# Optimization experiments

Hardware: AMD Instinct MI355X
Metric: run time of the kernel (lower is better)

## Reference

```python
import jax, jax.numpy as jnp
import numpy as np

B, S, E, H = 8, 1024, 1024, 16
D = E // H  # head_dim = 64


def setup_inputs() -> dict:
    key = jax.random.key(0)
    ks = jax.random.split(key, 8)
    scale = 1.0 / np.sqrt(E)
    return {
        "query": jax.random.normal(ks[0], (B, S, E), jnp.float32),
        "key": jax.random.normal(ks[1], (B, S, E), jnp.float32),
        "value": jax.random.normal(ks[2], (B, S, E), jnp.float32),
        "q_w": jax.random.normal(ks[3], (E, E), jnp.float32) * scale,
        "q_b": jnp.zeros((E,), jnp.float32),
        "k_w": jax.random.normal(ks[4], (E, E), jnp.float32) * scale,
        "k_b": jnp.zeros((E,), jnp.float32),
        "v_w": jax.random.normal(ks[5], (E, E), jnp.float32) * scale,
        "v_b": jnp.zeros((E,), jnp.float32),
        "out_w": jax.random.normal(ks[6], (E, E), jnp.float32) * scale,
        "out_b": jnp.zeros((E,), jnp.float32),
    }


def reference(query, key, value, q_w, q_b, k_w, k_b, v_w, v_b, out_w, out_b):
    b = query.shape[0]
    scaling = 1.0 / jnp.sqrt(jnp.asarray(D, query.dtype))
    # torch Linear: x @ W.T + b; split heads -> (b, H, S, D)
    def proj(x, w, bias):
        y = jnp.einsum('bse,fe->bsf', x, w) + bias
        return y.reshape(b, -1, H, D).transpose(0, 2, 1, 3)
    q = proj(query, q_w, q_b)
    k = proj(key, k_w, k_b)
    v = proj(value, v_w, v_b)
    scores = jnp.einsum('bhqd,bhkd->bhqk', q, k) * scaling
    attn_weights = jax.nn.softmax(scores, axis=-1)
    # dropout is identity in eval mode (deterministic reference)
    context = jnp.einsum('bhqk,bhkd->bhqd', attn_weights, v)
    context = context.transpose(0, 2, 1, 3).reshape(b, -1, E)
    output = jnp.einsum('bse,fe->bsf', context, out_w) + out_b
    return (attn_weights, output)
```

## Files before the change

kernel.cpp:

```cpp
#include <hip/hip_runtime.h>

typedef __attribute__((ext_vector_type(8))) short short8;
typedef __attribute__((ext_vector_type(4))) float f32x4;
typedef unsigned short u16;

#define DEVI __device__ __forceinline__

DEVI u16 f2bf(float f) {
  unsigned u = __float_as_uint(f);
  unsigned r = (u + 0x7fffu + ((u >> 16) & 1u)) >> 16;
  return (u16)r;
}

DEVI void gl2lds16(const void* g, void* l) {
  __builtin_amdgcn_global_load_lds((const __attribute__((address_space(1))) void*)g,
                                   (__attribute__((address_space(3))) void*)l, 16, 0, 0);
}

template<int ROWS, int BKE, int NT>
DEVI void stage_bf16(const u16* __restrict__ g, int ld, u16* lds, int tid) {
  constexpr int CPR = BKE / 8;
  constexpr int CH  = ROWS * CPR;
  constexpr int NW  = NT / 64;
  const int wave = tid >> 6, lane = tid & 63;
#pragma unroll
  for (int i = 0; i < CH / NT; i++) {
    int c = (i * NW + wave) * 64 + lane;
    int row = c / CPR;
    int colb = (c % CPR) * 16;
    gl2lds16((const char*)g + (long)row * ld * 2 + colb, (char*)lds + (long)c * 16);
  }
}

template<int FM, int FN, int BKE>
DEVI void kstep(const u16* Alds, const u16* Blds, int lane, int wr, int wc, int kk,
                f32x4 (*acc)[FN]) {
  const int ro = lane & 15, ko = kk + (lane >> 4) * 8;
  short8 a[FM], b[FN];
#pragma unroll
  for (int m = 0; m < FM; m++) a[m] = *(const short8*)(Alds + (wr + m * 16 + ro) * BKE + ko);
#pragma unroll
  for (int n = 0; n < FN; n++) b[n] = *(const short8*)(Blds + (wc + n * 16 + ro) * BKE + ko);
#pragma unroll
  for (int m = 0; m < FM; m++)
#pragma unroll
    for (int n = 0; n < FN; n++)
      acc[m][n] = __builtin_amdgcn_mfma_f32_16x16x32_bf16(a[m], b[n], acc[m][n], 0, 0, 0);
}

struct CvtArgs {
  const float* s[7];
  u16* d[7];
  int n8[7];
};

__global__ __launch_bounds__(256) void cvt_all(CvtArgs a) {
  const int t = blockIdx.y;
  const int n = a.n8[t];
  const float* __restrict__ s = a.s[t];
  u16* __restrict__ d = a.d[t];
  for (long i = blockIdx.x * 256 + threadIdx.x; i < n; i += (long)gridDim.x * 256) {
    float4 v0 = ((const float4*)s)[2 * i];
    float4 v1 = ((const float4*)s)[2 * i + 1];
    ushort4 h0, h1;
    h0.x = f2bf(v0.x); h0.y = f2bf(v0.y); h0.z = f2bf(v0.z); h0.w = f2bf(v0.w);
    h1.x = f2bf(v1.x); h1.y = f2bf(v1.y); h1.z = f2bf(v1.z); h1.w = f2bf(v1.w);
    ((ushort4*)d)[2 * i] = h0;
    ((ushort4*)d)[2 * i + 1] = h1;
  }
}

struct Biases { const float* p[3]; };

__global__ __launch_bounds__(256) void proj3_kernel(const u16* __restrict__ Xb,
                                                    const u16* __restrict__ Wb,
                                                    Biases bs,
                                                    u16* __restrict__ Outb) {
  __shared__ u16 Alds[128 * 64];
  __shared__ u16 Blds[128 * 64];
  const int tid = threadIdx.x, lane = tid & 63, w = tid >> 6;
  const int wr = (w >> 1) * 64, wc = (w & 1) * 64;
  const int z = blockIdx.z;
  const u16* X = Xb + (long)z * 8388608;
  const u16* W = Wb + (long)z * 1048576;
  const float* bias = bs.p[z];
  u16* Out = Outb + (long)z * 8388608;
  const long rowB = (long)blockIdx.x * 128;
  const int colB = blockIdx.y * 128;
  f32x4 acc[4][4] = {};
  for (int k0 = 0; k0 < 1024; k0 += 64) {
    stage_bf16<128, 64, 256>(X + rowB * 1024 + k0, 1024, Alds, tid);
    stage_bf16<128, 64, 256>(W + (long)colB * 1024 + k0, 1024, Blds, tid);
    __syncthreads();
    kstep<4, 4, 64>(Alds, Blds, lane, wr, wc, 0, acc);
    kstep<4, 4, 64>(Alds, Blds, lane, wr, wc, 32, acc);
    __syncthreads();
  }
  const int ro = (lane >> 4) * 4, co = lane & 15;
  const float sc = (z == 0) ? 0.125f : 1.0f;
  if (z < 2) {
#pragma unroll
    for (int n = 0; n < 4; n++) {
      const int col = colB + wc + n * 16 + co;
      const float bv = bias[col];
      const int h = col >> 6, d = col & 63;
#pragma unroll
      for (int m = 0; m < 4; m++)
#pragma unroll
        for (int j = 0; j < 4; j++) {
          long r = rowB + wr + m * 16 + ro + j;
          long bq = r >> 10, s = r & 1023;
          Out[(((bq * 16 + h) * 1024 + s) << 6) + d] = f2bf((acc[m][n][j] + bv) * sc);
        }
    }
  } else {
#pragma unroll
    for (int n = 0; n < 4; n++) {
      const int col = colB + wc + n * 16 + co;
      const float bv = bias[col];
      const long h = col >> 6, d = col & 63;
#pragma unroll
      for (int m = 0; m < 4; m++) {
        long r0 = rowB + wr + m * 16 + ro;
        long bq = r0 >> 10, s = r0 & 1023;
        ushort4 pk;
        pk.x = f2bf(acc[m][n][0] + bv);
        pk.y = f2bf(acc[m][n][1] + bv);
        pk.z = f2bf(acc[m][n][2] + bv);
        pk.w = f2bf(acc[m][n][3] + bv);
        *(ushort4*)(Out + (((bq * 16 + h) << 16) | (d << 10) | s)) = pk;
      }
    }
  }
}

__global__ __launch_bounds__(256) void flash_kernel(const u16* __restrict__ Q,
                                                    const u16* __restrict__ K,
                                                    const u16* __restrict__ Vt,
                                                    float* __restrict__ attn,
                                                    u16* __restrict__ Ctx) {
  __shared__ u16 lds[24576];
  u16* const Pl = lds + 16384;
  const int tid = threadIdx.x, lane = tid & 63, w = tid >> 6;
  const int z = blockIdx.x;
  const int rowB = blockIdx.y * 128;
  const int b = z >> 4, h = z & 15;
  const u16* Qb  = Q  + (long)z * 65536 + (long)rowB * 64;
  const u16* Kb  = K  + (long)z * 65536;
  const u16* Vtb = Vt + (long)z * 65536;
  const int ro = lane & 15, ko8 = (lane >> 4) * 8;
  const int qw = w * 32;

  short8 aq[2][2];
#pragma unroll
  for (int m = 0; m < 2; m++)
#pragma unroll
    for (int kt = 0; kt < 2; kt++)
      aq[m][kt] = *(const short8*)(Qb + (qw + m * 16 + ro) * 64 + kt * 32 + ko8);

  float lsum[8];
#pragma unroll
  for (int i = 0; i < 8; i++) lsum[i] = 0.0f;

  stage_bf16<128, 64, 256>(Kb, 64, lds, tid);
  __syncthreads();
  for (int kb = 0; kb < 8; kb++) {
    const int cur = kb & 1;
    if (kb < 7) stage_bf16<128, 64, 256>(Kb + (kb + 1) * 8192, 64, lds + ((kb + 1) & 1) * 8192, tid);
    const u16* Kc = lds + cur * 8192;
    f32x4 acc[2][8] = {};
    __builtin_amdgcn_s_setprio(1);
#pragma unroll
    for (int kt = 0; kt < 2; kt++) {
      short8 bfr[8];
#pragma unroll
      for (int n = 0; n < 8; n++)
        bfr[n] = *(const short8*)(Kc + (n * 16 + ro) * 64 + kt * 32 + ko8);
#pragma unroll
      for (int m = 0; m < 2; m++)
#pragma unroll
        for (int n = 0; n < 8; n++)
          acc[m][n] = __builtin_amdgcn_mfma_f32_16x16x32_bf16(aq[m][kt], bfr[n], acc[m][n], 0, 0, 0);
    }
    __builtin_amdgcn_s_setprio(0);
#pragma unroll
    for (int m = 0; m < 2; m++)
#pragma unroll
      for (int j = 0; j < 4; j++) {
        const int i = m * 4 + j;
        float e0 = __expf(acc[m][0][j]) + __expf(acc[m][1][j]) +
                   __expf(acc[m][2][j]) + __expf(acc[m][3][j]);
        float e1 = __expf(acc[m][4][j]) + __expf(acc[m][5][j]) +
                   __expf(acc[m][6][j]) + __expf(acc[m][7][j]);
        lsum[i] += e0 + e1;
      }
    __syncthreads();
  }

  stage_bf16<64, 64, 256>(Kb, 64, lds, tid);
  stage_bf16<64, 64, 256>(Vtb, 1024, lds + 8192, tid);
  float linv[8];
#pragma unroll
  for (int i = 0; i < 8; i++) {
    float s = lsum[i];
#pragma unroll
    for (int o = 8; o > 0; o >>= 1) s += __shfl_xor(s, o, 64);
    linv[i] = 1.0f / s;
  }
  __syncthreads();

  f32x4 acc_o[2][4] = {};
  float* ab = attn + ((long)z << 20) + (long)rowB * 1024;
  for (int kb = 0; kb < 16; kb++) {
    const int cur = kb & 1, nxt = cur ^ 1;
    if (kb < 15) {
      stage_bf16<64, 64, 256>(Kb + (kb + 1) * 4096, 64, lds + nxt * 4096, tid);
      stage_bf16<64, 64, 256>(Vtb + (kb + 1) * 64, 1024, lds + 8192 + nxt * 4096, tid);
    }
    const u16* Kc = lds + cur * 4096;
    const u16* Vc = lds + 8192 + cur * 4096;
    f32x4 acc[2][4] = {};
    __builtin_amdgcn_s_setprio(1);
#pragma unroll
    for (int kt = 0; kt < 2; kt++) {
      short8 bfr[4];
#pragma unroll
      for (int n = 0; n < 4; n++)
        bfr[n] = *(const short8*)(Kc + (n * 16 + ro) * 64 + kt * 32 + ko8);
#pragma unroll
      for (int m = 0; m < 2; m++)
#pragma unroll
        for (int n = 0; n < 4; n++)
          acc[m][n] = __builtin_amdgcn_mfma_f32_16x16x32_bf16(aq[m][kt], bfr[n], acc[m][n], 0, 0, 0);
    }
    __builtin_amdgcn_s_setprio(0);
#pragma unroll
    for (int m = 0; m < 2; m++)
#pragma unroll
      for (int j = 0; j < 4; j++) {
        const int i = m * 4 + j;
        const int ql = qw + m * 16 + (lane >> 4) * 4 + j;
        float* rowp = ab + (long)ql * 1024 + kb * 64;
        u16* prow = Pl + ql * 64;
        const int sw = ((ql & 7) << 3);
#pragma unroll
        for (int n = 0; n < 4; n++) {
          const int col = n * 16 + (lane & 15);
          float p = __expf(acc[m][n][j]) * linv[i];
          __builtin_nontemporal_store(p, rowp + col);
          prow[col ^ sw] = f2bf(p);
        }
      }
    asm volatile("s_waitcnt lgkmcnt(0)" ::: "memory");
    __builtin_amdgcn_sched_barrier(0);
    __builtin_amdgcn_s_setprio(1);
#pragma unroll
    for (int kt = 0; kt < 2; kt++) {
      short8 pa[2], bv[4];
#pragma unroll
      for (int m = 0; m < 2; m++) {
        const int row = qw + m * 16 + ro;
        pa[m] = *(const short8*)(Pl + row * 64 + ((kt * 32 + ko8) ^ ((row & 7) << 3)));
      }
#pragma unroll
      for (int n = 0; n < 4; n++)
        bv[n] = *(const short8*)(Vc + (n * 16 + ro) * 64 + kt * 32 + ko8);
#pragma unroll
      for (int m = 0; m < 2; m++)
#pragma unroll
        for (int n = 0; n < 4; n++)
          acc_o[m][n] = __builtin_amdgcn_mfma_f32_16x16x32_bf16(pa[m], bv[n], acc_o[m][n], 0, 0, 0);
    }
    __builtin_amdgcn_s_setprio(0);
    __syncthreads();
  }

  u16* cb = Ctx + ((long)b << 20) + (long)h * 64;
#pragma unroll
  for (int m = 0; m < 2; m++)
#pragma unroll
    for (int j = 0; j < 4; j++) {
      const long s = rowB + qw + m * 16 + (lane >> 4) * 4 + j;
#pragma unroll
      for (int n = 0; n < 4; n++)
        cb[s * 1024 + n * 16 + (lane & 15)] = f2bf(acc_o[m][n][j]);
    }
}

__global__ __launch_bounds__(256) void outb_kernel(const u16* __restrict__ Ctx,
                                                   const u16* __restrict__ W,
                                                   const float* __restrict__ bias,
                                                   float* __restrict__ Out) {
  __shared__ u16 Alds[128 * 64];
  __shared__ u16 Blds[128 * 64];
  const int tid = threadIdx.x, lane = tid & 63, w = tid >> 6;
  const int wr = (w >> 1) * 64, wc = (w & 1) * 64;
  const long rowB = (long)blockIdx.x * 128;
  const int colB = blockIdx.y * 128;
  f32x4 acc[4][4] = {};
  for (int k0 = 0; k0 < 1024; k0 += 64) {
    stage_bf16<128, 64, 256>(Ctx + rowB * 1024 + k0, 1024, Alds, tid);
    stage_bf16<128, 64, 256>(W + (long)colB * 1024 + k0, 1024, Blds, tid);
    __syncthreads();
    kstep<4, 4, 64>(Alds, Blds, lane, wr, wc, 0, acc);
    kstep<4, 4, 64>(Alds, Blds, lane, wr, wc, 32, acc);
    __syncthreads();
  }
  const int ro = (lane >> 4) * 4, co = lane & 15;
#pragma unroll
  for (int n = 0; n < 4; n++) {
    const int col = colB + wc + n * 16 + co;
    const float bv = bias[col];
#pragma unroll
    for (int m = 0; m < 4; m++)
#pragma unroll
      for (int j = 0; j < 4; j++) {
        long r = rowB + wr + m * 16 + ro + j;
        __builtin_nontemporal_store(acc[m][n][j] + bv, Out + r * 1024 + col);
      }
  }
}

extern "C" void kernel_launch(void* const* d_in, const int* in_sizes, int n_in,
                              void* d_out, int out_size, void* d_ws, size_t ws_size,
                              hipStream_t stream) {
  const float* query = (const float*)d_in[0];
  const float* key   = (const float*)d_in[1];
  const float* value = (const float*)d_in[2];
  const float* q_w   = (const float*)d_in[3];
  const float* q_b   = (const float*)d_in[4];
  const float* k_w   = (const float*)d_in[5];
  const float* k_b   = (const float*)d_in[6];
  const float* v_w   = (const float*)d_in[7];
  const float* v_b   = (const float*)d_in[8];
  const float* out_w = (const float*)d_in[9];
  const float* out_b = (const float*)d_in[10];

  const long MB = 1048576L;
  char* ws = (char*)d_ws;
  u16* Qp  = (u16*)(ws);
  u16* Kp  = (u16*)(ws + 16 * MB);
  u16* Vt  = (u16*)(ws + 32 * MB);
  u16* Qb  = (u16*)(ws + 48 * MB);
  u16* Kb  = (u16*)(ws + 64 * MB);
  u16* Vb  = (u16*)(ws + 80 * MB);
  u16* Ctx = (u16*)(ws + 64 * MB);
  u16* Wq  = (u16*)(ws + 96 * MB);
  u16* Wk  = (u16*)(ws + 98 * MB);
  u16* Wv  = (u16*)(ws + 100 * MB);
  u16* Wo  = (u16*)(ws + 102 * MB);

  float* attn = (float*)d_out;
  float* outp = (float*)d_out + 134217728L;

  CvtArgs ca;
  ca.s[0] = query; ca.d[0] = Qb; ca.n8[0] = 1048576;
  ca.s[1] = key;   ca.d[1] = Kb; ca.n8[1] = 1048576;
  ca.s[2] = value; ca.d[2] = Vb; ca.n8[2] = 1048576;
  ca.s[3] = q_w;   ca.d[3] = Wq; ca.n8[3] = 131072;
  ca.s[4] = k_w;   ca.d[4] = Wk; ca.n8[4] = 131072;
  ca.s[5] = v_w;   ca.d[5] = Wv; ca.n8[5] = 131072;
  ca.s[6] = out_w; ca.d[6] = Wo; ca.n8[6] = 131072;

  Biases bs;
  bs.p[0] = q_b; bs.p[1] = k_b; bs.p[2] = v_b;

  cvt_all<<<dim3(2048, 7), dim3(256), 0, stream>>>(ca);
  proj3_kernel<<<dim3(64, 8, 3), dim3(256), 0, stream>>>(Qb, Wq, bs, Qp);
  flash_kernel<<<dim3(128, 8), dim3(256), 0, stream>>>(Qp, Kp, Vt, attn, Ctx);
  outb_kernel<<<dim3(64, 8), dim3(256), 0, stream>>>(Ctx, Wo, out_b, outp);
}
```

Before: 337.7 us.

## Load K and V fragments directly from global memory in flash kernel

Removes the double-buffered LDS staging of K and transposed V in both passes of the attention kernel. Each wave now reads its MFMA B-operand fragments straight from global memory and relies on L1/L2 to serve the reuse across waves. This drops all block-level barriers and shrinks shared memory to just the per-wave P buffer, which should allow more resident blocks and let waves overlap their attention-weight stores better. The cost is roughly four times more global/cache load traffic for K and V, and the load latency is no longer hidden by explicit prefetch.

```diff
diff --git a/kernel.cpp b/kernel.cpp
--- a/kernel.cpp
+++ b/kernel.cpp
@@ -139,8 +139,7 @@
                                                     const u16* __restrict__ Vt,
                                                     float* __restrict__ attn,
                                                     u16* __restrict__ Ctx) {
-  __shared__ u16 lds[24576];
-  u16* const Pl = lds + 16384;
+  __shared__ u16 Pl[8192];
   const int tid = threadIdx.x, lane = tid & 63, w = tid >> 6;
   const int z = blockIdx.x;
   const int rowB = blockIdx.y * 128;
@@ -162,24 +161,20 @@
 #pragma unroll
   for (int i = 0; i < 8; i++) lsum[i] = 0.0f;
 
-  stage_bf16<128, 64, 256>(Kb, 64, lds, tid);
-  __syncthreads();
-  for (int kb = 0; kb < 8; kb++) {
-    const int cur = kb & 1;
-    if (kb < 7) stage_bf16<128, 64, 256>(Kb + (kb + 1) * 8192, 64, lds + ((kb + 1) & 1) * 8192, tid);
-    const u16* Kc = lds + cur * 8192;
-    f32x4 acc[2][8] = {};
+  for (int kb = 0; kb < 16; kb++) {
+    const u16* Kt = Kb + kb * 4096;
+    f32x4 acc[2][4] = {};
     __builtin_amdgcn_s_setprio(1);
 #pragma unroll
     for (int kt = 0; kt < 2; kt++) {
-      short8 bfr[8];
-#pragma unroll
-      for (int n = 0; n < 8; n++)
-        bfr[n] = *(const short8*)(Kc + (n * 16 + ro) * 64 + kt * 32 + ko8);
+      short8 bfr[4];
+#pragma unroll
+      for (int n = 0; n < 4; n++)
+        bfr[n] = *(const short8*)(Kt + (n * 16 + ro) * 64 + kt * 32 + ko8);
 #pragma unroll
       for (int m = 0; m < 2; m++)
 #pragma unroll
-        for (int n = 0; n < 8; n++)
+        for (int n = 0; n < 4; n++)
           acc[m][n] = __builtin_amdgcn_mfma_f32_16x16x32_bf16(aq[m][kt], bfr[n], acc[m][n], 0, 0, 0);
     }
     __builtin_amdgcn_s_setprio(0);
@@ -188,17 +183,10 @@
 #pragma unroll
       for (int j = 0; j < 4; j++) {
         const int i = m * 4 + j;
-        float e0 = __expf(acc[m][0][j]) + __expf(acc[m][1][j]) +
+        lsum[i] += __expf(acc[m][0][j]) + __expf(acc[m][1][j]) +
                    __expf(acc[m][2][j]) + __expf(acc[m][3][j]);
-        float e1 = __expf(acc[m][4][j]) + __expf(acc[m][5][j]) +
-                   __expf(acc[m][6][j]) + __expf(acc[m][7][j]);
-        lsum[i] += e0 + e1;
-      }
-    __syncthreads();
-  }
-
-  stage_bf16<64, 64, 256>(Kb, 64, lds, tid);
-  stage_bf16<64, 64, 256>(Vtb, 1024, lds + 8192, tid);
+      }
+  }
   float linv[8];
 #pragma unroll
   for (int i = 0; i < 8; i++) {
@@ -207,18 +195,11 @@
     for (int o = 8; o > 0; o >>= 1) s += __shfl_xor(s, o, 64);
     linv[i] = 1.0f / s;
   }
-  __syncthreads();
 
   f32x4 acc_o[2][4] = {};
   float* ab = attn + ((long)z << 20) + (long)rowB * 1024;
   for (int kb = 0; kb < 16; kb++) {
-    const int cur = kb & 1, nxt = cur ^ 1;
-    if (kb < 15) {
-      stage_bf16<64, 64, 256>(Kb + (kb + 1) * 4096, 64, lds + nxt * 4096, tid);
-      stage_bf16<64, 64, 256>(Vtb + (kb + 1) * 64, 1024, lds + 8192 + nxt * 4096, tid);
-    }
-    const u16* Kc = lds + cur * 4096;
-    const u16* Vc = lds + 8192 + cur * 4096;
+    const u16* Kt = Kb + kb * 4096;
     f32x4 acc[2][4] = {};
     __builtin_amdgcn_s_setprio(1);
 #pragma unroll
@@ -226,7 +207,7 @@
       short8 bfr[4];
 #pragma unroll
       for (int n = 0; n < 4; n++)
-        bfr[n] = *(const short8*)(Kc + (n * 16 + ro) * 64 + kt * 32 + ko8);
+        bfr[n] = *(const short8*)(Kt + (n * 16 + ro) * 64 + kt * 32 + ko8);
 #pragma unroll
       for (int m = 0; m < 2; m++)
 #pragma unroll
@@ -264,7 +245,7 @@
       }
 #pragma unroll
       for (int n = 0; n < 4; n++)
-        bv[n] = *(const short8*)(Vc + (n * 16 + ro) * 64 + kt * 32 + ko8);
+        bv[n] = *(const short8*)(Vtb + (n * 16 + ro) * 1024 + kb * 64 + kt * 32 + ko8);
 #pragma unroll
       for (int m = 0; m < 2; m++)
 #pragma unroll
@@ -272,7 +253,6 @@
           acc_o[m][n] = __builtin_amdgcn_mfma_f32_16x16x32_bf16(pa[m], bv[n], acc_o[m][n], 0, 0, 0);
     }
     __builtin_amdgcn_s_setprio(0);
-    __syncthreads();
   }
 
   u16* cb = Ctx + ((long)b << 20) + (long)h * 64;
```

New measurement: 376.8 us. +11.6%, slower.
